# Performance work log

Measured on AMD Instinct MI355X. Metric: run time of the kernel, lower is better.

## Reference

```python
import jax, jax.numpy as jnp
import numpy as np
from jax import lax

AR_VOCAB = 25
EN_VOCAB = 25
N_CLASSES = 1 + AR_VOCAB + EN_VOCAB + AR_VOCAB * EN_VOCAB  # full_table id layout
NEG = -jnp.inf
BIG_NEG = -1e30  # acts as log(0) in float32 (exp underflows to exactly 0) but keeps grads finite
T_LEN = 256
V_LEN = 256


def setup_inputs() -> dict:
    key = jax.random.key(0)
    k1, k2 = jax.random.split(key)
    ar_sent = jax.random.randint(k1, (1, T_LEN), 0, AR_VOCAB)
    en_sent = jax.random.randint(k2, (1, V_LEN), 0, EN_VOCAB)
    # self.weights = log(uniform) over target classes
    weights = jnp.full((N_CLASSES,), -jnp.log(jnp.float32(N_CLASSES)), dtype=jnp.float32)
    return {"ar_sent": ar_sent, "en_sent": en_sent, "weights": weights}


def _chain(c, m):
    """Solve a[0]=c[0]; a[i]=logaddexp(c[i], m[i]+a[i-1]) in parallel.
    a[i] = s[i] + logcumsumexp(c - s)[i] with s = prefix sums of m (s[0]=0)."""
    s = jnp.concatenate([jnp.zeros((1,), c.dtype), jnp.cumsum(m[1:])])
    return s + lax.associative_scan(jnp.logaddexp, c - s)


def _safe_lse(x, axis):
    """Stable logsumexp that returns -inf (with zero gradient) on empty/-inf slices."""
    m = lax.stop_gradient(jnp.max(x, axis=axis, keepdims=True))
    m = jnp.where(jnp.isfinite(m), m, 0.0)
    s = jnp.sum(jnp.exp(x - m), axis=axis)
    ok = s > 0
    return jnp.squeeze(m, axis=axis) + jnp.where(ok, jnp.log(jnp.where(ok, s, 1.0)), NEG)


def _forward(ar, en, weights):
    # ar: [T] int, en: [V] int, weights: [C] log-probs
    T, V = ar.shape[0], en.shape[0]
    del_ids = 1 + ar                                               # [T]
    ins_ids = 1 + AR_VOCAB + en                                    # [V]
    sub_ids = 1 + AR_VOCAB + EN_VOCAB + EN_VOCAB * ar[:, None] + en[None, :]  # [T,V]
    w_del = weights[del_ids]   # [T]
    w_ins = weights[ins_ids]   # [V]
    w_sub = weights[sub_ids]   # [T,V]

    # ---- alpha DP (forward lattice) ----
    # row 0: alpha[0,0]=0, alpha[0,v]=alpha[0,v-1]+w_ins[v]
    c0 = jnp.full((V,), BIG_NEG, weights.dtype).at[0].set(0.0)
    row0 = _chain(c0, w_ins)

    def fstep(prev, xs):
        wd, ws = xs  # w_del[t] scalar, w_sub[t,:] [V]
        # c[v] = logaddexp(w_del[t]+alpha[t-1,v], w_sub[t,v]+alpha[t-1,v-1]); v=0 has no sub term
        c = jnp.concatenate([(wd + prev[0])[None],
                             jnp.logaddexp(wd + prev[1:], ws[1:] + prev[:-1])])
        row = _chain(c, w_ins)  # adds within-row insertion recurrence
        return row, row

    _, frows = lax.scan(fstep, row0, (w_del[1:], w_sub[1:]))
    alpha = jnp.concatenate([row0[None], frows], axis=0)  # [T,V]

    # ---- beta DP (backward lattice) ----
    m_rev = w_ins[::-1]
    cT = jnp.full((V,), BIG_NEG, weights.dtype).at[-1].set(0.0)
    rowT = _chain(cT[::-1], m_rev)[::-1]

    def bstep(nxt, xs):
        wd, ws = xs
        # c[v] = logaddexp(w_del[t]+beta[t+1,v], w_sub[t,v]+beta[t+1,v+1]); v=V-1 has no sub term
        c = jnp.concatenate([jnp.logaddexp(wd + nxt[:-1], ws[:-1] + nxt[1:]),
                             (wd + nxt[-1])[None]])
        row = _chain(c[::-1], m_rev)[::-1]  # beta[t,v] += w_ins[v]+beta[t,v+1] recurrence
        return row, row

    _, brows = lax.scan(bstep, rowT, (w_del[:-1], w_sub[:-1]), reverse=True)
    beta = jnp.concatenate([brows, rowT[None]], axis=0)  # [T,V]

    # ---- expected edit-operation counts (log space) ----
    cls = jnp.arange(N_CLASSES)
    w = weights[None, None, :]
    md = jnp.where(del_ids[1:, None, None] == cls, 0.0, NEG)   # [T-1,1,C] one-hot log mask
    mi = jnp.where(ins_ids[None, 1:, None] == cls, 0.0, NEG)   # [1,V-1,C]
    ms = jnp.where(sub_ids[1:, 1:, None] == cls, 0.0, NEG)     # [T-1,V-1,C]
    ed = alpha[:-1, :, None] + w + md + beta[1:, :, None]      # expected deletions
    ei = alpha[:, :-1, None] + w + mi + beta[:, 1:, None]      # expected insertions
    es = alpha[:-1, :-1, None] + w + ms + beta[1:, 1:, None]   # expected substitutions
    return _safe_lse(jnp.stack([_safe_lse(ed, (0, 1)),
                                _safe_lse(ei, (0, 1)),
                                _safe_lse(es, (0, 1))]), 0)    # [C]


def reference(ar_sent, en_sent, weights):
    return _forward(ar_sent[0], en_sent[0], weights)
```

## Files before the change

kernel.cpp:

```cpp
#include <hip/hip_runtime.h>
#include <math.h>

#define NCLS 676
#define NEG_SENTINEL -3.0e38f
#define LN2F 0.6931471805599453f
#define JPAD 768
#define RS 256
#define QIP_OFF 692
#define WSE_OFF (QIP_OFF + JPAD)
#define CTL_PROG 20692
#define CTL_CONS 20693
#define SLOT_OFF 20696
#define SHM_TOT 20720
#define MAGIC 0x13579BDFu
#define NSLICE 8

__device__ __forceinline__ float dpp_shr1(float x) {
  return __int_as_float(
      __builtin_amdgcn_update_dpp(0, __float_as_int(x), 0x138, 0xF, 0xF, false));
}
__device__ __forceinline__ float dpp_shl1(float x) {
  return __int_as_float(
      __builtin_amdgcn_update_dpp(0, __float_as_int(x), 0x130, 0xF, 0xF, false));
}
__device__ __forceinline__ int dpp_shr1_i(int x) {
  return __builtin_amdgcn_update_dpp(0, x, 0x138, 0xF, 0xF, false);
}
__device__ __forceinline__ int dpp_shl1_i(int x) {
  return __builtin_amdgcn_update_dpp(0, x, 0x130, 0xF, 0xF, false);
}
__device__ __forceinline__ float pow2c(int d) {
  d = min(max(d, -126), 126);
  return __int_as_float((d + 127) << 23);
}

__global__ __launch_bounds__(256, 1) void k_dp(const int* __restrict__ ar,
                                               const int* __restrict__ en,
                                               const float* __restrict__ wts,
                                               float* __restrict__ aD,
                                               float* __restrict__ bD,
                                               int* __restrict__ aEb,
                                               int* __restrict__ bEb,
                                               float* __restrict__ S,
                                               unsigned* __restrict__ flags) {
  const int tid = threadIdx.x;
  __shared__ alignas(16) float shm[SHM_TOT];

  float* pw = shm;
  int* progp = (int*)(shm + CTL_PROG);
  int* consp = (int*)(shm + CTL_CONS);
  for (int c = tid; c < NCLS; c += 256) pw[c] = __expf(wts[c]);
  {
    float4* z = (float4*)(shm + NCLS);
    const int nz = (SHM_TOT - NCLS) / 4;
    for (int t = tid; t < nz; t += 256) z[t] = make_float4(0.f, 0.f, 0.f, 0.f);
  }
  if (tid == 0) { *progp = 0; *consp = 0; }
  if (blockIdx.x == 0) {
    for (int c = tid; c < NSLICE * NCLS; c += 256) S[c] = 0.f;
    if (tid == 0)
      __hip_atomic_store(&flags[2], 0u, __ATOMIC_RELAXED,
                         __HIP_MEMORY_SCOPE_AGENT);
  }
  __syncthreads();
  {
    int j = tid;
    int ee = en[j];
    shm[QIP_OFF + 255 + j] = pw[26 + ee];
#pragma unroll
    for (int a = 0; a < 25; ++a)
      shm[WSE_OFF + a * JPAD + 255 + j] = pw[51 + 25 * a + ee];
  }
  __syncthreads();
  const int wid = tid >> 6;
  const int lane = tid & 63;
  if (wid >= 2) return;

  const int i0 = 2 * lane + 128 * wid;
  float wdl[2];
  int roff[2];
#pragma unroll
  for (int k = 0; k < 2; ++k) {
    int a = ar[i0 + k];
    wdl[k] = pw[1 + a];
    roff[k] = WSE_OFF + a * JPAD;
  }
  float P1[2] = {0.f, 0.f};
  float P2[2] = {0.f, 0.f};
  int e1 = 0;

#define LOAD_A2(EB)                                                        \
  {                                                                        \
    _Pragma("unroll") for (int k = 0; k < 2; ++k) {                        \
      const int bo = roff[k] + (EB);                                       \
      float2 va = *(const float2*)&shm[bo];                                \
      float2 vb = *(const float2*)&shm[bo + 2];                            \
      float2 vc = *(const float2*)&shm[bo + 4];                            \
      float2 vd = *(const float2*)&shm[bo + 6];                            \
      float2 ve = *(const float2*)&shm[bo + 8];                            \
      float2 vf = *(const float2*)&shm[bo + 10];                           \
      W[k][0] = va.x; W[k][1] = va.y; W[k][2] = vb.x; W[k][3] = vb.y;      \
      W[k][4] = vc.x; W[k][5] = vc.y; W[k][6] = vd.x; W[k][7] = vd.y;      \
      W[k][8] = ve.x; W[k][9] = ve.y; W[k][10] = vf.x; W[k][11] = vf.y;    \
    }                                                                      \
    const int qo = QIP_OFF + (EB);                                         \
    float2 qa = *(const float2*)&shm[qo];                                  \
    float2 qb = *(const float2*)&shm[qo + 2];                              \
    float2 qc = *(const float2*)&shm[qo + 4];                              \
    float2 qd = *(const float2*)&shm[qo + 6];                              \
    float2 qe = *(const float2*)&shm[qo + 8];                              \
    float2 qf = *(const float2*)&shm[qo + 10];                             \
    Q[0] = qa.x; Q[1] = qa.y; Q[2] = qb.x; Q[3] = qb.y; Q[4] = qc.x;       \
    Q[5] = qc.y; Q[6] = qd.x; Q[7] = qd.y; Q[8] = qe.x; Q[9] = qe.y;       \
    Q[10] = qf.x; Q[11] = qf.y;                                            \
  }

#define LOAD_B2(EB)                                                        \
  {                                                                        \
    _Pragma("unroll") for (int k = 0; k < 2; ++k) {                        \
      const int bo = roff[k] + (EB);                                       \
      float2 va = *(const float2*)&shm[bo];                                \
      float2 vb = *(const float2*)&shm[bo + 2];                            \
      float2 vc = *(const float2*)&shm[bo + 4];                            \
      float2 vd = *(const float2*)&shm[bo + 6];                            \
      float2 ve = *(const float2*)&shm[bo + 8];                            \
      float2 vf = *(const float2*)&shm[bo + 10];                           \
      float2 vg = *(const float2*)&shm[bo + 12];                           \
      float2 vh = *(const float2*)&shm[bo + 14];                           \
      W[k][0] = va.x; W[k][1] = va.y; W[k][2] = vb.x; W[k][3] = vb.y;      \
      W[k][4] = vc.x; W[k][5] = vc.y; W[k][6] = vd.x; W[k][7] = vd.y;      \
      W[k][8] = ve.x; W[k][9] = ve.y; W[k][10] = vf.x; W[k][11] = vf.y;    \
      W[k][12] = vg.x; W[k][13] = vg.y; W[k][14] = vh.x; W[k][15] = vh.y;  \
    }                                                                      \
    const int qo = QIP_OFF + (EB);                                         \
    float2 qa = *(const float2*)&shm[qo];                                  \
    float2 qb = *(const float2*)&shm[qo + 2];                              \
    float2 qc = *(const float2*)&shm[qo + 4];                              \
    float2 qd = *(const float2*)&shm[qo + 6];                              \
    float2 qe = *(const float2*)&shm[qo + 8];                              \
    float2 qf = *(const float2*)&shm[qo + 10];                             \
    float2 qg = *(const float2*)&shm[qo + 12];                             \
    float2 qh = *(const float2*)&shm[qo + 14];                             \
    Q[0] = qa.x; Q[1] = qa.y; Q[2] = qb.x; Q[3] = qb.y; Q[4] = qc.x;       \
    Q[5] = qc.y; Q[6] = qd.x; Q[7] = qd.y; Q[8] = qe.x; Q[9] = qe.y;       \
    Q[10] = qf.x; Q[11] = qf.y; Q[12] = qg.x; Q[13] = qg.y; Q[14] = qh.x;  \
    Q[15] = qh.y;                                                          \
  }

  if (blockIdx.x == 0) {
    if (wid == 0) {
      if (lane == 0) { P1[0] = 1.f; aD[255] = 1.f; }
      int e0 = 252 - i0;
      float* sp = aD + RS + 254 - i0;
      int* ep = aEb + i0;
      float W[2][12], Q[12];
      LOAD_A2(e0);
      for (int p = 0; p < 64; ++p) {
        const int e1st = e1;
        int t1e = dpp_shr1_i(e1);
        float f1n = pow2c(t1e - e1);
        float pmc = dpp_shr1(P2[1]) * f1n;
        float cs[8][2];
#pragma unroll
        for (int u = 0; u < 8; ++u) {
          float pm1 = dpp_shr1(P1[1]) * f1n;
          float pm2 = pmc;
          float c0 = fmaf(wdl[0], pm1, fmaf(W[0][4 + u], pm2, Q[4 + u] * P1[0]));
          float c1 = fmaf(wdl[1], P1[0], fmaf(W[1][3 + u], P2[0], Q[3 + u] * P1[1]));
          cs[u][0] = c0; cs[u][1] = c1;
          P2[0] = P1[0]; P2[1] = P1[1]; P1[0] = c0; P1[1] = c1;
          pmc = pm1;
        }
        if (lane == 63) {
          while (__hip_atomic_load(consp, __ATOMIC_RELAXED,
                                   __HIP_MEMORY_SCOPE_WORKGROUP) < p - 1) {}
          float* sl = shm + SLOT_OFF + (p & 1) * 12;
          *(float4*)(sl) = make_float4(cs[0][1], cs[1][1], cs[2][1], cs[3][1]);
          *(float4*)(sl + 4) = make_float4(cs[4][1], cs[5][1], cs[6][1], cs[7][1]);
          ((int*)sl)[8] = e1st;
          __hip_atomic_store(progp, p + 1, __ATOMIC_RELEASE,
                             __HIP_MEMORY_SCOPE_WORKGROUP);
        }
#pragma unroll
        for (int u = 0; u < 8; ++u) {
          *(float2*)sp = make_float2(cs[u][1], cs[u][0]);
          sp += RS;
        }
        e0 += 8;
        LOAD_A2(e0);
        float m = fmaxf(P1[0], P1[1]);
        int ex = (m > 0.f) ? ((__float_as_int(m) >> 23) - 126) : (t1e - e1);
        float sc = pow2c(-ex);
        P1[0] *= sc; P1[1] *= sc; P2[0] *= sc; P2[1] *= sc;
        e1 += ex;
        *(int2*)ep = make_int2(e1st, e1st); ep += 256;
      }
    } else {
      int e0 = 252 - i0;
      float* sp = aD + RS + 254 - i0;
      int* ep = aEb + i0;
      float W[2][12], Q[12];
      LOAD_A2(e0);
      float t1raw = 0.f, t2raw = 0.f;
      int eBprev = 0;
      const bool isL0 = (lane == 0);
      for (int p = 0; p < 64; ++p) {
        while (__hip_atomic_load(progp, __ATOMIC_ACQUIRE,
                                 __HIP_MEMORY_SCOPE_WORKGROUP) < p + 1) {}
        const float* sl = shm + SLOT_OFF + (p & 1) * 12;
        float4 r0 = *(const float4*)sl;
        float4 r1 = *(const float4*)(sl + 4);
        int eB = ((const int*)sl)[8];
        float scm = isL0 ? pow2c(eB - e1) : 0.f;
        float spm = isL0 ? pow2c(eBprev - e1) : 0.f;
        float B1[8];
        B1[0] = t1raw * spm;
        B1[1] = r0.x * scm; B1[2] = r0.y * scm; B1[3] = r0.z * scm;
        B1[4] = r0.w * scm; B1[5] = r1.x * scm; B1[6] = r1.y * scm;
        B1[7] = r1.z * scm;
        float B2s = t2raw * spm;
        t1raw = r1.w; t2raw = r1.z; eBprev = eB;
        const int e1st = e1;
        int td = dpp_shr1_i(e1);
        int t1e = isL0 ? eB : td;
        float f1n = pow2c(t1e - e1);
        float pmc = fmaf(dpp_shr1(P2[1]), f1n, B2s);
        float cs[8][2];
#pragma unroll
        for (int u = 0; u < 8; ++u) {
          float pm1 = fmaf(dpp_shr1(P1[1]), f1n, B1[u]);
          float pm2 = pmc;
          float c0 = fmaf(wdl[0], pm1, fmaf(W[0][4 + u], pm2, Q[4 + u] * P1[0]));
          float c1 = fmaf(wdl[1], P1[0], fmaf(W[1][3 + u], P2[0], Q[3 + u] * P1[1]));
          cs[u][0] = c0; cs[u][1] = c1;
          P2[0] = P1[0]; P2[1] = P1[1]; P1[0] = c0; P1[1] = c1;
          pmc = pm1;
        }
#pragma unroll
        for (int u = 0; u < 8; ++u) {
          *(float2*)sp = make_float2(cs[u][1], cs[u][0]);
          sp += RS;
        }
        e0 += 8;
        LOAD_A2(e0);
        float m = fmaxf(P1[0], P1[1]);
        int ex = (m > 0.f) ? ((__float_as_int(m) >> 23) - 126) : (t1e - e1);
        float sc = pow2c(-ex);
        P1[0] *= sc; P1[1] *= sc; P2[0] *= sc; P2[1] *= sc;
        e1 += ex;
        *(int2*)ep = make_int2(e1st, e1st); ep += 256;
        if (isL0)
          __hip_atomic_store(consp, p + 1, __ATOMIC_RELEASE,
                             __HIP_MEMORY_SCOPE_WORKGROUP);
      }
      {
        int pe = 252 - i0;
        for (int pp = 0; pp < 128; ++pp) {
          const int EBp = pe & 255;
          LOAD_A2(EBp);
#pragma unroll
          for (int x = 0; x < 12; ++x)
            asm volatile("" ::"v"(W[0][x]), "v"(W[1][x]), "v"(Q[x]));
          pe += 8;
        }
      }
      __threadfence();
      if (lane == 0)
        __hip_atomic_store(&flags[0], MAGIC, __ATOMIC_RELEASE,
                           __HIP_MEMORY_SCOPE_AGENT);
    }
  } else {
    if (wid == 1) {
      if (lane == 63) P1[1] = 1.f;
      if (lane == 0) bD[510 * RS] = 1.f;
      int e0 = 764 - i0;
      float* sp = bD + 509 * RS + 254 - i0;
      int* ep = bEb + i0;
      float W[2][16], Q[16];
      LOAD_B2(e0);
      for (int p = 0; p < 64; ++p) {
        const int e1st = e1;
        int t1e = dpp_shl1_i(e1);
        float f1n = pow2c(t1e - e1);
        float pmc = dpp_shl1(P2[0]) * f1n;
        float cs[8][2];
#pragma unroll
        for (int u = 0; u < 8; ++u) {
          float pm1 = dpp_shl1(P1[0]) * f1n;
          float pm2 = pmc;
          float c1 = fmaf(wdl[1], pm1, fmaf(W[1][11 - u], pm2, Q[12 - u] * P1[1]));
          float c0 = fmaf(wdl[0], P1[1], fmaf(W[0][12 - u], P2[1], Q[13 - u] * P1[0]));
          cs[u][0] = c0; cs[u][1] = c1;
          P2[0] = P1[0]; P2[1] = P1[1]; P1[0] = c0; P1[1] = c1;
          pmc = pm1;
        }
        if (lane == 0) {
          while (__hip_atomic_load(consp, __ATOMIC_RELAXED,
                                   __HIP_MEMORY_SCOPE_WORKGROUP) < p - 1) {}
          float* sl = shm + SLOT_OFF + (p & 1) * 12;
          *(float4*)(sl) = make_float4(cs[0][0], cs[1][0], cs[2][0], cs[3][0]);
          *(float4*)(sl + 4) = make_float4(cs[4][0], cs[5][0], cs[6][0], cs[7][0]);
          ((int*)sl)[8] = e1st;
          __hip_atomic_store(progp, p + 1, __ATOMIC_RELEASE,
                             __HIP_MEMORY_SCOPE_WORKGROUP);
        }
#pragma unroll
        for (int u = 0; u < 8; ++u) {
          *(float2*)sp = make_float2(cs[u][1], cs[u][0]);
          sp -= RS;
        }
        e0 -= 8;
        LOAD_B2(e0);
        float m = fmaxf(P1[0], P1[1]);
        int ex = (m > 0.f) ? ((__float_as_int(m) >> 23) - 126) : (t1e - e1);
        float sc = pow2c(-ex);
        P1[0] *= sc; P1[1] *= sc; P2[0] *= sc; P2[1] *= sc;
        e1 += ex;
        *(int2*)ep = make_int2(e1st, e1st); ep += 256;
      }
    } else {
      int e0 = 764 - i0;
      float* sp = bD + 509 * RS + 254 - i0;
      int* ep = bEb + i0;
      float W[2][16], Q[16];
      LOAD_B2(e0);
      float t1raw = 0.f, t2raw = 0.f;
      int eBprev = 0;
      const bool isT = (lane == 63);
      for (int p = 0; p < 64; ++p) {
        while (__hip_atomic_load(progp, __ATOMIC_ACQUIRE,
                                 __HIP_MEMORY_SCOPE_WORKGROUP) < p + 1) {}
        const float* sl = shm + SLOT_OFF + (p & 1) * 12;
        float4 r0 = *(const float4*)sl;
        float4 r1 = *(const float4*)(sl + 4);
        int eB = ((const int*)sl)[8];
        float scm = isT ? pow2c(eB - e1) : 0.f;
        float spm = isT ? pow2c(eBprev - e1) : 0.f;
        float B1[8];
        B1[0] = t1raw * spm;
        B1[1] = r0.x * scm; B1[2] = r0.y * scm; B1[3] = r0.z * scm;
        B1[4] = r0.w * scm; B1[5] = r1.x * scm; B1[6] = r1.y * scm;
        B1[7] = r1.z * scm;
        float B2s = t2raw * spm;
        t1raw = r1.w; t2raw = r1.z; eBprev = eB;
        const int e1st = e1;
        int td = dpp_shl1_i(e1);
        int t1e = isT ? eB : td;
        float f1n = pow2c(t1e - e1);
        float pmc = fmaf(dpp_shl1(P2[0]), f1n, B2s);
        float cs[8][2];
#pragma unroll
        for (int u = 0; u < 8; ++u) {
          float pm1 = fmaf(dpp_shl1(P1[0]), f1n, B1[u]);
          float pm2 = pmc;
          float c1 = fmaf(wdl[1], pm1, fmaf(W[1][11 - u], pm2, Q[12 - u] * P1[1]));
          float c0 = fmaf(wdl[0], P1[1], fmaf(W[0][12 - u], P2[1], Q[13 - u] * P1[0]));
          cs[u][0] = c0; cs[u][1] = c1;
          P2[0] = P1[0]; P2[1] = P1[1]; P1[0] = c0; P1[1] = c1;
          pmc = pm1;
        }
#pragma unroll
        for (int u = 0; u < 8; ++u) {
          *(float2*)sp = make_float2(cs[u][1], cs[u][0]);
          sp -= RS;
        }
        e0 -= 8;
        LOAD_B2(e0);
        float m = fmaxf(P1[0], P1[1]);
        int ex = (m > 0.f) ? ((__float_as_int(m) >> 23) - 126) : (t1e - e1);
        float sc = pow2c(-ex);
        P1[0] *= sc; P1[1] *= sc; P2[0] *= sc; P2[1] *= sc;
        e1 += ex;
        *(int2*)ep = make_int2(e1st, e1st); ep += 256;
        if (isT)
          __hip_atomic_store(consp, p + 1, __ATOMIC_RELEASE,
                             __HIP_MEMORY_SCOPE_WORKGROUP);
      }
      __threadfence();
      if (lane == 0)
        __hip_atomic_store(&flags[1], MAGIC, __ATOMIC_RELEASE,
                           __HIP_MEMORY_SCOPE_AGENT);
    }
  }
}

__global__ __launch_bounds__(256) void k_red(const int* __restrict__ ar,
                                             const int* __restrict__ en,
                                             const float* __restrict__ wts,
                                             const float* __restrict__ aD,
                                             const float* __restrict__ bD,
                                             const int* __restrict__ aEb,
                                             const int* __restrict__ bEb,
                                             float* __restrict__ S,
                                             unsigned* __restrict__ flags,
                                             float* __restrict__ out) {
  const int tid = threadIdx.x;
  __shared__ float bins[NCLS];
  __shared__ int ctl;
  for (int c = tid; c < NCLS; c += 256) bins[c] = 0.f;
  __syncthreads();
  const float M = __logf(aD[510 * RS]) +
                  (float)aEb[63 * 256 + 255] * LN2F + 16.0f;
  const int j = tid;
  const int e = en[j];
#pragma unroll
  for (int u = 0; u < 4; ++u) {
    const int d = (int)blockIdx.x * 4 + u;
    if (d <= 510) {
      const int i = d - j;
      if (i >= 0 && i <= 255) {
        const float bM = bD[d * RS + 255 - i];
        if (bM > 0.f) {
          const int bEx =
              (d == 510) ? 0 : bEb[((509 - d) >> 3) * 256 + i];
          const float lb = __logf(bM) + (float)bEx * LN2F - M;
          const int a = ar[i];
          if (i >= 1) {
            float aM = aD[(d - 1) * RS + 256 - i];
            if (aM > 0.f) {
              int eA = (d == 1) ? 0 : aEb[((d - 2) >> 3) * 256 + (i - 1)];
              float L = __logf(aM) + (float)eA * LN2F + lb;
              atomicAdd(&bins[1 + a], __expf(fminf(L, 0.f)));
            }
          }
          if (j >= 1) {
            float aM = aD[(d - 1) * RS + 255 - i];
            if (aM > 0.f) {
              int eA = (d == 1) ? 0 : aEb[((d - 2) >> 3) * 256 + i];
              float L = __logf(aM) + (float)eA * LN2F + lb;
              atomicAdd(&bins[26 + e], __expf(fminf(L, 0.f)));
            }
            if (i >= 1) {
              float aM2 = aD[(d - 2) * RS + 256 - i];
              if (aM2 > 0.f) {
                int eA2 = (d == 2) ? 0 : aEb[((d - 3) >> 3) * 256 + (i - 1)];
                float L2 = __logf(aM2) + (float)eA2 * LN2F + lb;
                atomicAdd(&bins[51 + 25 * a + e], __expf(fminf(L2, 0.f)));
              }
            }
          }
        }
      }
    }
  }
  __syncthreads();
  float* Ss = S + (blockIdx.x & (NSLICE - 1)) * NCLS;
  for (int c = tid; c < NCLS; c += 256)
    if (bins[c] != 0.f) atomicAdd(&Ss[c], bins[c]);
  __syncthreads();
  if (tid == 0) {
    unsigned n = __hip_atomic_fetch_add(&flags[2], 1u, __ATOMIC_ACQ_REL,
                                        __HIP_MEMORY_SCOPE_AGENT);
    ctl = ((n & 127u) == 127u);
  }
  __syncthreads();
  if (ctl) {
    for (int c = tid; c < NCLS; c += 256) {
      float s = 0.f;
#pragma unroll
      for (int q = 0; q < NSLICE; ++q)
        s += __hip_atomic_load(&S[q * NCLS + c], __ATOMIC_RELAXED,
                               __HIP_MEMORY_SCOPE_AGENT);
      out[c] = (c != 0 && s > 0.f) ? (wts[c] + M + __logf(s)) : NEG_SENTINEL;
    }
  }
}

extern "C" void kernel_launch(void* const* d_in, const int* in_sizes, int n_in,
                              void* d_out, int out_size, void* d_ws, size_t ws_size,
                              hipStream_t stream) {
  const int* ar = (const int*)d_in[0];
  const int* en = (const int*)d_in[1];
  const float* wts = (const float*)d_in[2];
  float* aD = (float*)d_ws;
  float* bDraw = aD + 514 * RS;
  float* bD = bDraw + 2 * RS;
  int* aEb = (int*)(bDraw + 514 * RS);
  int* bEb = aEb + 64 * 256;
  float* S = (float*)(bEb + 64 * 256);
  unsigned* flags = (unsigned*)(S + NSLICE * NCLS);
  k_dp<<<2, 256, 0, stream>>>(ar, en, wts, aD, bD, aEb, bEb, S, flags);
  k_red<<<128, 256, 0, stream>>>(ar, en, wts, aD, bD, aEb, bEb, S, flags,
                                 (float*)d_out);
}
```

Before: 113.8 us.

## Fuse DP and reduction kernels with progress flags for overlapped consumption

Merges the two-block DP kernel and the 128-block reduction kernel into one 130-block launch. DP waves publish per-8-step progress counters, so reduction blocks can load and log-transform their diagonals as soon as those rows exist, then wait only for the final normaliser before accumulating. It also drops a dummy reload loop and resets the flags with a memset. This risks deadlock if all blocks are not co-resident, and adds spin-polling traffic plus threadfences in the DP critical loop.

```diff
diff --git a/kernel.cpp b/kernel.cpp
--- a/kernel.cpp
+++ b/kernel.cpp
@@ -34,17 +34,131 @@
   return __int_as_float((d + 127) << 23);
 }
 
-__global__ __launch_bounds__(256, 1) void k_dp(const int* __restrict__ ar,
-                                               const int* __restrict__ en,
-                                               const float* __restrict__ wts,
-                                               float* __restrict__ aD,
-                                               float* __restrict__ bD,
-                                               int* __restrict__ aEb,
-                                               int* __restrict__ bEb,
-                                               float* __restrict__ S,
-                                               unsigned* __restrict__ flags) {
+__global__ __launch_bounds__(256, 1) void k_fused(const int* __restrict__ ar,
+                                                  const int* __restrict__ en,
+                                                  const float* __restrict__ wts,
+                                                  float* __restrict__ aD,
+                                                  float* __restrict__ bD,
+                                                  int* __restrict__ aEb,
+                                                  int* __restrict__ bEb,
+                                                  float* __restrict__ S,
+                                                  unsigned* __restrict__ flags,
+                                                  float* __restrict__ out) {
   const int tid = threadIdx.x;
   __shared__ alignas(16) float shm[SHM_TOT];
+
+  if (blockIdx.x >= 2) {
+    float* bins = shm;
+    for (int c = tid; c < NCLS; c += 256) bins[c] = 0.f;
+    __syncthreads();
+    const int dbase = 4 * ((int)blockIdx.x - 2);
+    const int dmaxv = min(dbase + 3, 510);
+    const unsigned cA = (unsigned)max(1, min(8, (dmaxv - 1 + 63) / 64));
+    const unsigned cB = (unsigned)max(1, min(8, (510 - dbase + 63) / 64));
+    if (tid == 0) {
+      while (__hip_atomic_load(&flags[3], __ATOMIC_RELAXED,
+                               __HIP_MEMORY_SCOPE_AGENT) < cA ||
+             __hip_atomic_load(&flags[4], __ATOMIC_RELAXED,
+                               __HIP_MEMORY_SCOPE_AGENT) < cA ||
+             __hip_atomic_load(&flags[5], __ATOMIC_RELAXED,
+                               __HIP_MEMORY_SCOPE_AGENT) < cB ||
+             __hip_atomic_load(&flags[6], __ATOMIC_RELAXED,
+                               __HIP_MEMORY_SCOPE_AGENT) < cB)
+        __builtin_amdgcn_s_sleep(8);
+      (void)__hip_atomic_load(&flags[3], __ATOMIC_ACQUIRE,
+                              __HIP_MEMORY_SCOPE_AGENT);
+    }
+    __syncthreads();
+    const int j = tid;
+    const int e = en[j];
+    float S1[4], S2[4], S3[4];
+    int C1[4], C3[4];
+#pragma unroll
+    for (int u = 0; u < 4; ++u) {
+      S1[u] = NEG_SENTINEL; S2[u] = NEG_SENTINEL; S3[u] = NEG_SENTINEL;
+      C1[u] = 0; C3[u] = 0;
+      const int d = dbase + u;
+      if (d <= 510) {
+        const int i = d - j;
+        if (i >= 0 && i <= 255) {
+          const float bM = bD[d * RS + 255 - i];
+          if (bM > 0.f) {
+            const int bEx =
+                (d == 510) ? 0 : bEb[((509 - d) >> 3) * 256 + i];
+            const float lb = __logf(bM) + (float)bEx * LN2F;
+            const int a = ar[i];
+            C1[u] = 1 + a;
+            C3[u] = 51 + 25 * a + e;
+            if (i >= 1) {
+              float aM = aD[(d - 1) * RS + 256 - i];
+              if (aM > 0.f) {
+                int eA = (d == 1) ? 0 : aEb[((d - 2) >> 3) * 256 + (i - 1)];
+                S1[u] = __logf(aM) + (float)eA * LN2F + lb;
+              }
+            }
+            if (j >= 1) {
+              float aM = aD[(d - 1) * RS + 255 - i];
+              if (aM > 0.f) {
+                int eA = (d == 1) ? 0 : aEb[((d - 2) >> 3) * 256 + i];
+                S2[u] = __logf(aM) + (float)eA * LN2F + lb;
+              }
+              if (i >= 1) {
+                float aM2 = aD[(d - 2) * RS + 256 - i];
+                if (aM2 > 0.f) {
+                  int eA2 = (d == 2) ? 0 : aEb[((d - 3) >> 3) * 256 + (i - 1)];
+                  S3[u] = __logf(aM2) + (float)eA2 * LN2F + lb;
+                }
+              }
+            }
+          }
+        }
+      }
+    }
+    if (tid == 0) {
+      while (__hip_atomic_load(&flags[0], __ATOMIC_RELAXED,
+                               __HIP_MEMORY_SCOPE_AGENT) != MAGIC ||
+             __hip_atomic_load(&flags[1], __ATOMIC_RELAXED,
+                               __HIP_MEMORY_SCOPE_AGENT) != MAGIC)
+        __builtin_amdgcn_s_sleep(8);
+      (void)__hip_atomic_load(&flags[0], __ATOMIC_ACQUIRE,
+                              __HIP_MEMORY_SCOPE_AGENT);
+    }
+    __syncthreads();
+    const float M = __logf(aD[510 * RS]) +
+                    (float)aEb[63 * 256 + 255] * LN2F + 16.0f;
+#pragma unroll
+    for (int u = 0; u < 4; ++u) {
+      if (S1[u] > -1.0e30f)
+        atomicAdd(&bins[C1[u]], __expf(fminf(S1[u] - M, 0.f)));
+      if (S2[u] > -1.0e30f)
+        atomicAdd(&bins[26 + e], __expf(fminf(S2[u] - M, 0.f)));
+      if (S3[u] > -1.0e30f)
+        atomicAdd(&bins[C3[u]], __expf(fminf(S3[u] - M, 0.f)));
+    }
+    __syncthreads();
+    float* Ss = S + ((int)blockIdx.x & (NSLICE - 1)) * NCLS;
+    for (int c = tid; c < NCLS; c += 256)
+      if (bins[c] != 0.f) atomicAdd(&Ss[c], bins[c]);
+    __syncthreads();
+    __shared__ int ctlw;
+    if (tid == 0) {
+      unsigned n = __hip_atomic_fetch_add(&flags[2], 1u, __ATOMIC_ACQ_REL,
+                                          __HIP_MEMORY_SCOPE_AGENT);
+      ctlw = ((n & 127u) == 127u);
+    }
+    __syncthreads();
+    if (ctlw) {
+      for (int c = tid; c < NCLS; c += 256) {
+        float s = 0.f;
+#pragma unroll
+        for (int q = 0; q < NSLICE; ++q)
+          s += __hip_atomic_load(&S[q * NCLS + c], __ATOMIC_RELAXED,
+                                 __HIP_MEMORY_SCOPE_AGENT);
+        out[c] = (c != 0 && s > 0.f) ? (wts[c] + M + __logf(s)) : NEG_SENTINEL;
+      }
+    }
+    return;
+  }
 
   float* pw = shm;
   int* progp = (int*)(shm + CTL_PROG);
@@ -56,12 +170,8 @@
     for (int t = tid; t < nz; t += 256) z[t] = make_float4(0.f, 0.f, 0.f, 0.f);
   }
   if (tid == 0) { *progp = 0; *consp = 0; }
-  if (blockIdx.x == 0) {
+  if (blockIdx.x == 0)
     for (int c = tid; c < NSLICE * NCLS; c += 256) S[c] = 0.f;
-    if (tid == 0)
-      __hip_atomic_store(&flags[2], 0u, __ATOMIC_RELAXED,
-                         __HIP_MEMORY_SCOPE_AGENT);
-  }
   __syncthreads();
   {
     int j = tid;
@@ -147,6 +257,14 @@
     Q[15] = qh.y;                                                          \
   }
 
+#define PUBLISH(FID)                                                       \
+  if ((p & 7) == 7) {                                                      \
+    __threadfence();                                                       \
+    if (lane == 0)                                                         \
+      __hip_atomic_store(&flags[FID], (unsigned)((p >> 3) + 1),            \
+                         __ATOMIC_RELEASE, __HIP_MEMORY_SCOPE_AGENT);      \
+  }
+
   if (blockIdx.x == 0) {
     if (wid == 0) {
       if (lane == 0) { P1[0] = 1.f; aD[255] = 1.f; }
@@ -194,6 +312,7 @@
         P1[0] *= sc; P1[1] *= sc; P2[0] *= sc; P2[1] *= sc;
         e1 += ex;
         *(int2*)ep = make_int2(e1st, e1st); ep += 256;
+        PUBLISH(3)
       }
     } else {
       int e0 = 252 - i0;
@@ -252,17 +371,7 @@
         if (isL0)
           __hip_atomic_store(consp, p + 1, __ATOMIC_RELEASE,
                              __HIP_MEMORY_SCOPE_WORKGROUP);
-      }
-      {
-        int pe = 252 - i0;
-        for (int pp = 0; pp < 128; ++pp) {
-          const int EBp = pe & 255;
-          LOAD_A2(EBp);
-#pragma unroll
-          for (int x = 0; x < 12; ++x)
-            asm volatile("" ::"v"(W[0][x]), "v"(W[1][x]), "v"(Q[x]));
-          pe += 8;
-        }
+        PUBLISH(4)
       }
       __threadfence();
       if (lane == 0)
@@ -317,6 +426,7 @@
         P1[0] *= sc; P1[1] *= sc; P2[0] *= sc; P2[1] *= sc;
         e1 += ex;
         *(int2*)ep = make_int2(e1st, e1st); ep += 256;
+        PUBLISH(5)
       }
     } else {
       int e0 = 764 - i0;
@@ -375,93 +485,12 @@
         if (isT)
           __hip_atomic_store(consp, p + 1, __ATOMIC_RELEASE,
                              __HIP_MEMORY_SCOPE_WORKGROUP);
+        PUBLISH(6)
       }
       __threadfence();
       if (lane == 0)
         __hip_atomic_store(&flags[1], MAGIC, __ATOMIC_RELEASE,
                            __HIP_MEMORY_SCOPE_AGENT);
-    }
-  }
-}
-
-__global__ __launch_bounds__(256) void k_red(const int* __restrict__ ar,
-                                             const int* __restrict__ en,
-                                             const float* __restrict__ wts,
-                                             const float* __restrict__ aD,
-                                             const float* __restrict__ bD,
-                                             const int* __restrict__ aEb,
-                                             const int* __restrict__ bEb,
-                                             float* __restrict__ S,
-                                             unsigned* __restrict__ flags,
-                                             float* __restrict__ out) {
-  const int tid = threadIdx.x;
-  __shared__ float bins[NCLS];
-  __shared__ int ctl;
-  for (int c = tid; c < NCLS; c += 256) bins[c] = 0.f;
-  __syncthreads();
-  const float M = __logf(aD[510 * RS]) +
-                  (float)aEb[63 * 256 + 255] * LN2F + 16.0f;
-  const int j = tid;
-  const int e = en[j];
-#pragma unroll
-  for (int u = 0; u < 4; ++u) {
-    const int d = (int)blockIdx.x * 4 + u;
-    if (d <= 510) {
-      const int i = d - j;
-      if (i >= 0 && i <= 255) {
-        const float bM = bD[d * RS + 255 - i];
-        if (bM > 0.f) {
-          const int bEx =
-              (d == 510) ? 0 : bEb[((509 - d) >> 3) * 256 + i];
-          const float lb = __logf(bM) + (float)bEx * LN2F - M;
-          const int a = ar[i];
-          if (i >= 1) {
-            float aM = aD[(d - 1) * RS + 256 - i];
-            if (aM > 0.f) {
-              int eA = (d == 1) ? 0 : aEb[((d - 2) >> 3) * 256 + (i - 1)];
-              float L = __logf(aM) + (float)eA * LN2F + lb;
-              atomicAdd(&bins[1 + a], __expf(fminf(L, 0.f)));
-            }
-          }
-          if (j >= 1) {
-            float aM = aD[(d - 1) * RS + 255 - i];
-            if (aM > 0.f) {
-              int eA = (d == 1) ? 0 : aEb[((d - 2) >> 3) * 256 + i];
-              float L = __logf(aM) + (float)eA * LN2F + lb;
-              atomicAdd(&bins[26 + e], __expf(fminf(L, 0.f)));
-            }
-            if (i >= 1) {
-              float aM2 = aD[(d - 2) * RS + 256 - i];
-              if (aM2 > 0.f) {
-                int eA2 = (d == 2) ? 0 : aEb[((d - 3) >> 3) * 256 + (i - 1)];
-                float L2 = __logf(aM2) + (float)eA2 * LN2F + lb;
-                atomicAdd(&bins[51 + 25 * a + e], __expf(fminf(L2, 0.f)));
-              }
-            }
-          }
-        }
-      }
-    }
-  }
-  __syncthreads();
-  float* Ss = S + (blockIdx.x & (NSLICE - 1)) * NCLS;
-  for (int c = tid; c < NCLS; c += 256)
-    if (bins[c] != 0.f) atomicAdd(&Ss[c], bins[c]);
-  __syncthreads();
-  if (tid == 0) {
-    unsigned n = __hip_atomic_fetch_add(&flags[2], 1u, __ATOMIC_ACQ_REL,
-                                        __HIP_MEMORY_SCOPE_AGENT);
-    ctl = ((n & 127u) == 127u);
-  }
-  __syncthreads();
-  if (ctl) {
-    for (int c = tid; c < NCLS; c += 256) {
-      float s = 0.f;
-#pragma unroll
-      for (int q = 0; q < NSLICE; ++q)
-        s += __hip_atomic_load(&S[q * NCLS + c], __ATOMIC_RELAXED,
-                               __HIP_MEMORY_SCOPE_AGENT);
-      out[c] = (c != 0 && s > 0.f) ? (wts[c] + M + __logf(s)) : NEG_SENTINEL;
     }
   }
 }
@@ -479,7 +508,7 @@
   int* bEb = aEb + 64 * 256;
   float* S = (float*)(bEb + 64 * 256);
   unsigned* flags = (unsigned*)(S + NSLICE * NCLS);
-  k_dp<<<2, 256, 0, stream>>>(ar, en, wts, aD, bD, aEb, bEb, S, flags);
-  k_red<<<128, 256, 0, stream>>>(ar, en, wts, aD, bD, aEb, bEb, S, flags,
-                                 (float*)d_out);
-}
+  hipMemsetAsync((void*)flags, 0, 7 * sizeof(unsigned), stream);
+  k_fused<<<130, 256, 0, stream>>>(ar, en, wts, aD, bD, aEb, bEb, S, flags,
+                                   (float*)d_out);
+}
```

Measured after the change: 107.6 us. 1.06x faster.
